# Optimization experiments

Measured on AMD Instinct MI355X. Metric: run time of the kernel, lower is better.

The kernel has to match this reference:

```python
import jax, jax.numpy as jnp
import numpy as np

N, E = 50000, 800000
IN, MAP, H, O = 256, 64, 4, 64
LEAKY_SLOPE = 0.2


def setup_inputs() -> dict:
    key = jax.random.key(0)
    ks = jax.random.split(key, 12)
    x = jax.random.normal(ks[0], (N, IN), dtype=jnp.float32)
    src = jax.random.randint(ks[1], (E,), 0, N, dtype=jnp.int32)
    dst = jax.random.randint(ks[2], (E,), 0, N, dtype=jnp.int32)
    s = 1.0 / np.sqrt(IN)
    W_gat = jax.random.normal(ks[3], (IN, H * O), dtype=jnp.float32) * s
    attn_l = jax.random.normal(ks[4], (H, O), dtype=jnp.float32) * 0.1
    attn_r = jax.random.normal(ks[5], (H, O), dtype=jnp.float32) * 0.1
    gate_m_W = jax.random.normal(ks[6], (IN, MAP), dtype=jnp.float32) * s
    gate_m_b = jnp.zeros((MAP,), dtype=jnp.float32)
    gate_fn_W = jax.random.normal(ks[7], (2 * IN + MAP, H), dtype=jnp.float32) * (1.0 / np.sqrt(2 * IN + MAP))
    gate_fn_b = jnp.zeros((H,), dtype=jnp.float32)
    merge_W = jax.random.normal(ks[8], (IN + O, O), dtype=jnp.float32) * (1.0 / np.sqrt(IN + O))
    merge_b = jnp.zeros((O,), dtype=jnp.float32)
    return {"x": x, "src": src, "dst": dst, "W_gat": W_gat, "attn_l": attn_l,
            "attn_r": attn_r, "gate_m_W": gate_m_W, "gate_m_b": gate_m_b,
            "gate_fn_W": gate_fn_W, "gate_fn_b": gate_fn_b,
            "merge_W": merge_W, "merge_b": merge_b}


def _forward(x, src, dst, W_gat, attn_l, attn_r, gate_m_W, gate_m_b,
             gate_fn_W, gate_fn_b, merge_W, merge_b):
    n = x.shape[0]
    # --- gate branch: gspmm mean of x, gspmm max of linear_z over in-neighbors ---
    deg = jax.ops.segment_sum(jnp.ones_like(dst, dtype=x.dtype), dst, num_segments=n)
    mean_z = jax.ops.segment_sum(x[src], dst, num_segments=n) / jnp.maximum(deg, 1.0)[:, None]
    z = x @ gate_m_W + gate_m_b  # [N, MAP]
    max_z = jax.ops.segment_max(z[src], dst, num_segments=n)
    max_z = jnp.where(deg[:, None] > 0, max_z, 0.0)  # empty neighborhoods -> 0
    nft = jnp.concatenate([x, max_z, mean_z], axis=1)  # [N, 2*IN+MAP]
    gate = jax.nn.sigmoid(nft @ gate_fn_W + gate_fn_b)  # [N, H]
    # --- GATConv ---
    feat = (x @ W_gat).reshape(n, H, O)  # [N, H, O]
    el = jnp.einsum('nho,ho->nh', feat, attn_l)
    er = jnp.einsum('nho,ho->nh', feat, attn_r)
    e = jax.nn.leaky_relu(el[src] + er[dst], negative_slope=LEAKY_SLOPE)  # [E, H]
    m = jax.ops.segment_max(e, dst, num_segments=n)  # [N, H]
    m = jnp.where(jnp.isfinite(m), m, 0.0)
    ex = jnp.exp(e - m[dst])  # [E, H]
    s = jax.ops.segment_sum(ex, dst, num_segments=n)  # [N, H]
    alpha = ex / jnp.maximum(s[dst], 1e-16)  # [E, H]
    attn_out = jax.ops.segment_sum(feat[src] * alpha[:, :, None], dst, num_segments=n)  # [N, H, O]
    # --- gated merge ---
    gated = (gate[:, :, None] * attn_out).mean(axis=1)  # [N, O]
    merge = jnp.concatenate([x, gated], axis=1) @ merge_W + merge_b  # [N, O]
    return merge


def reference(x, src, dst, W_gat, attn_l, attn_r, gate_m_W, gate_m_b,
              gate_fn_W, gate_fn_b, merge_W, merge_b):
    return _forward(x, src, dst, W_gat, attn_l, attn_r, gate_m_W, gate_m_b,
                    gate_fn_W, gate_fn_b, merge_W, merge_b)
```

## Files before the change

kernel.cpp:

```cpp
#include <hip/hip_runtime.h>
#include <math.h>

#define NN 50000
#define NE 800000
#define LEAKY 0.2f
#define NT 26
#define CAP 96
#define NBT (8 * NT * 64)

typedef short bf16x8 __attribute__((ext_vector_type(8)));
typedef float f32x4 __attribute__((ext_vector_type(4)));
typedef float f32x2 __attribute__((ext_vector_type(2)));

__device__ __forceinline__ unsigned short f2bf(float f) {
  unsigned u = __float_as_uint(f);
  u += 0x7fffu + ((u >> 16) & 1u);
  return (unsigned short)(u >> 16);
}
__device__ __forceinline__ float bf2f(unsigned short h) {
  return __uint_as_float((unsigned)h << 16);
}
__device__ __forceinline__ float leaky(float v) { return v > 0.0f ? v : LEAKY * v; }
__device__ __forceinline__ float rlf(float v, int l) {
  return __uint_as_float(__builtin_amdgcn_readlane(__float_as_uint(v), l));
}
__device__ __forceinline__ int rli(int v, int l) {
  return __builtin_amdgcn_readlane(v, l);
}

#if defined(__has_builtin)
#if __has_builtin(__builtin_amdgcn_cvt_pk_f32_fp8) && \
    __has_builtin(__builtin_amdgcn_cvt_pk_fp8_f32) && \
    __has_builtin(__builtin_amdgcn_cvt_f32_fp8)
#define FP8_HW 1
#endif
#endif

#ifdef FP8_HW
__device__ __forceinline__ unsigned char f2fp8(float v) {
  return (unsigned char)(__builtin_amdgcn_cvt_pk_fp8_f32(v, v, 0u, false) & 0xFF);
}
__device__ __forceinline__ f32x2 fp8x2_lo(unsigned int v) {
  return __builtin_amdgcn_cvt_pk_f32_fp8(v, false);
}
__device__ __forceinline__ f32x2 fp8x2_hi(unsigned int v) {
  return __builtin_amdgcn_cvt_pk_f32_fp8(v, true);
}
__device__ __forceinline__ float fp8one(unsigned int v) {
  return __builtin_amdgcn_cvt_f32_fp8(v, 0);
}
#else
__device__ __forceinline__ unsigned char f2fp8(float f) {
  unsigned u = __float_as_uint(f);
  unsigned s = (u >> 31) << 7;
  unsigned a = u & 0x7FFFFFFFu;
  if (a >= 0x43E00000u) return (unsigned char)(s | 0x7E);
  if (a < 0x3C800000u) {
    float m = __uint_as_float(a) * 512.0f;
    int q = (int)(m + 0.5f); if (q > 7) q = 7;
    return (unsigned char)(s | q);
  }
  a += 0x7FFFFu + ((a >> 20) & 1);
  unsigned e = ((a >> 23) & 0xFF) - 120;
  if (e > 15) return (unsigned char)(s | 0x7E);
  return (unsigned char)(s | (e << 3) | ((a >> 20) & 7));
}
__device__ __forceinline__ float fp8dec1(unsigned b) {
  unsigned s = (b & 0x80u) << 24;
  unsigned em = b & 0x7Fu;
  unsigned e4 = em >> 3, m3 = em & 7;
  float v = e4 ? __uint_as_float(((e4 + 120) << 23) | (m3 << 20))
               : (float)m3 * 0.001953125f;
  return __uint_as_float(__float_as_uint(v) ^ s);
}
__device__ __forceinline__ f32x2 fp8x2_lo(unsigned int v) {
  f32x2 r;
  r[0] = fp8dec1(v & 0xFF);
  r[1] = fp8dec1((v >> 8) & 0xFF);
  return r;
}
__device__ __forceinline__ f32x2 fp8x2_hi(unsigned int v) {
  f32x2 r;
  r[0] = fp8dec1((v >> 16) & 0xFF);
  r[1] = fp8dec1((v >> 24) & 0xFF);
  return r;
}
__device__ __forceinline__ float fp8one(unsigned int v) { return fp8dec1(v & 0xFF); }
#endif

__global__ void k_init(int* __restrict__ cursor, unsigned char* __restrict__ zq,
                       float* __restrict__ epay) {
  int i = blockIdx.x * 256 + threadIdx.x;
  if (i < NN) cursor[i] = 0;
  if (blockIdx.x == 0) {
    int t = threadIdx.x;
    if (t < 64) zq[(size_t)NN * 64 + t] = 0xFE;
    if (t < 8) epay[(size_t)NN * 8 + t] = 0.0f;
  }
}

__global__ void k_scatter(const int* __restrict__ src, const int* __restrict__ dst,
                          int* __restrict__ cursor, int* __restrict__ csr_src) {
  int e = blockIdx.x * 256 + threadIdx.x;
  if (e < NE) {
    int n = dst[e];
    int pos = atomicAdd(&cursor[n], 1);
    if (pos < CAP) csr_src[n * CAP + pos] = src[e];
  }
}

__device__ __forceinline__ float panel_w(int col, int k,
    const float* W_gat, const float* gate_m_W, const float* merge_W,
    const float* gate_fn_W) {
  if (col < 256)      return W_gat[k * 256 + (col & 3) * 64 + (col >> 2)];
  else if (col < 320) return gate_m_W[k * 64 + (col - 256)];
  else if (col < 384) return merge_W[k * 64 + (col - 320)];
  else if (col < 388) return gate_fn_W[k * 4 + (col - 384)];
  else if (col < 392) return gate_fn_W[(320 + k) * 4 + (col - 388)];
  return 0.0f;
}

__global__ void k_bt(const float* __restrict__ W_gat, const float* __restrict__ gate_m_W,
                     const float* __restrict__ merge_W, const float* __restrict__ gate_fn_W,
                     unsigned short* __restrict__ Btf, unsigned short* __restrict__ mWf) {
  int idx = blockIdx.x * 256 + threadIdx.x;
  if (idx < NBT) {
    int kq = idx / (NT * 64);
    int rem = idx - kq * (NT * 64);
    int t = rem >> 6, lane = rem & 63;
    int col = t * 16 + (lane & 15);
    int k = kq * 32 + (lane >> 4) * 8;
    unsigned short* o = Btf + (size_t)idx * 8;
#pragma unroll
    for (int i = 0; i < 8; ++i)
      o[i] = f2bf(panel_w(col, k + i, W_gat, gate_m_W, merge_W, gate_fn_W));
  } else if (idx < NBT + 512) {
    int idx2 = idx - NBT;
    int kq = idx2 >> 8;
    int rem = idx2 & 255;
    int t = rem >> 6, lane = rem & 63;
    int col = t * 16 + (lane & 15);
    int k = kq * 32 + ((lane >> 4) & 3) * 8;
    unsigned short* o = mWf + (size_t)idx2 * 8;
#pragma unroll
    for (int i = 0; i < 8; ++i)
      o[i] = f2bf(merge_W[(size_t)(256 + k + i) * 64 + col]);
  }
}

__global__ __launch_bounds__(256) void k_gemm_mfma(
    const float* __restrict__ x, const unsigned short* __restrict__ Btf,
    const float* __restrict__ gate_m_b,
    const float* __restrict__ attn_l, const float* __restrict__ attn_r,
    unsigned char* __restrict__ featq, unsigned char* __restrict__ zq,
    float* __restrict__ xm, float* __restrict__ gx, float* __restrict__ epay,
    float* __restrict__ erv) {
  __shared__ float els[32][4][2];
  __shared__ float ers[32][4][2];
  int lane = threadIdx.x & 63;
  int wave = threadIdx.x >> 6;
  int rowHalf = wave >> 1, colHalf = wave & 1;
  int rowB = blockIdx.x * 32;
  int row0 = rowB + rowHalf * 16;
  int t0 = colHalf * 13;
  int m = lane & 15;
  int kg = lane >> 4;
  f32x4 zero = {0.f, 0.f, 0.f, 0.f};
  f32x4 acc[13];
#pragma unroll
  for (int t = 0; t < 13; ++t) acc[t] = zero;
  int arow = row0 + m; if (arow >= NN) arow = NN - 1;
  const float* apf = x + (size_t)arow * 256 + kg * 8;
#pragma unroll 1
  for (int kq = 0; kq < 8; ++kq) {
    float4 fa = *(const float4*)(apf + kq * 32);
    float4 fb = *(const float4*)(apf + kq * 32 + 4);
    bf16x8 a;
    a[0] = (short)f2bf(fa.x); a[1] = (short)f2bf(fa.y);
    a[2] = (short)f2bf(fa.z); a[3] = (short)f2bf(fa.w);
    a[4] = (short)f2bf(fb.x); a[5] = (short)f2bf(fb.y);
    a[6] = (short)f2bf(fb.z); a[7] = (short)f2bf(fb.w);
    bf16x8 bfr[13];
#pragma unroll
    for (int t = 0; t < 13; ++t)
      bfr[t] = *(const bf16x8*)(Btf + (((size_t)kq * NT + t0 + t) * 64 + lane) * 8);
#pragma unroll
    for (int t = 0; t < 13; ++t)
      acc[t] = __builtin_amdgcn_mfma_f32_16x16x32_bf16(a, bfr[t], acc[t], 0, 0, 0);
  }

  int h = m & 3, od = m >> 2;
  float elp[4] = {0, 0, 0, 0}, erp[4] = {0, 0, 0, 0};
#pragma unroll
  for (int t = 0; t < 13; ++t) {
    if ((t0 + t) * 16 < 256) {
      int o = (t0 + t) * 4 + od;
      float al = attn_l[h * 64 + o];
      float ar = attn_r[h * 64 + o];
#pragma unroll
      for (int r = 0; r < 4; ++r) {
        elp[r] += acc[t][r] * al;
        erp[r] += acc[t][r] * ar;
      }
    }
  }
#pragma unroll
  for (int r = 0; r < 4; ++r) {
    elp[r] += __shfl_xor(elp[r], 4, 64); elp[r] += __shfl_xor(elp[r], 8, 64);
    erp[r] += __shfl_xor(erp[r], 4, 64); erp[r] += __shfl_xor(erp[r], 8, 64);
  }
  if (m < 4) {
#pragma unroll
    for (int r = 0; r < 4; ++r) {
      els[rowHalf * 16 + kg * 4 + r][m][colHalf] = elp[r];
      ers[rowHalf * 16 + kg * 4 + r][m][colHalf] = erp[r];
    }
  }

#pragma unroll
  for (int r = 0; r < 4; ++r) {
    int row = row0 + kg * 4 + r;
    if (row >= NN) continue;
#pragma unroll
    for (int t = 0; t < 13; ++t) {
      int c = (t0 + t) * 16 + m;
      float val = acc[t][r];
      if (c < 256) {
        featq[(size_t)row * 256 + c] = f2fp8(val);
      } else if (c < 320) {
        int cc = c - 256;
        zq[(size_t)row * 64 + cc] = f2fp8(val + gate_m_b[cc]);
      } else if (c < 384) {
        xm[(size_t)row * 64 + (c - 320)] = val;
      } else if (c < 388) {
        gx[(size_t)row * 4 + (c - 384)] = val;
      } else if (c < 392) {
        epay[(size_t)row * 8 + (c - 388) + 4] = val;
      }
    }
  }
  __syncthreads();
  int tid = threadIdx.x;
  if (tid < 128) {
    int rr = tid >> 2, h2 = tid & 3;
    int row = rowB + rr;
    if (row < NN) {
      epay[(size_t)row * 8 + h2] = els[rr][h2][0] + els[rr][h2][1];
      erv[(size_t)row * 4 + h2] = ers[rr][h2][0] + ers[rr][h2][1];
    }
  }
}

__global__ __launch_bounds__(256) void k_node(
    const unsigned char* __restrict__ zq, const unsigned char* __restrict__ featq,
    const float* __restrict__ epay, const float* __restrict__ er,
    const float* __restrict__ gx,
    const int* __restrict__ cursor, const int* __restrict__ csr_src,
    const float* __restrict__ gate_fn_W, const float* __restrict__ gate_fn_b,
    unsigned short* __restrict__ gatedb) {
  __shared__ float WzT[4][64];
  int tid = threadIdx.x;
  {
    int c = tid >> 2, h = tid & 3;
    WzT[h][c] = gate_fn_W[(256 + c) * 4 + h];
  }
  __syncthreads();

  int lane = tid & 63;
  int node = blockIdx.x * 4 + (tid >> 6);
  if (node >= NN) return;
  int deg = cursor[node]; if (deg > CAP) deg = CAP;
  if (deg == 0) {
    gatedb[(size_t)node * 64 + lane] = 0;
    return;
  }
  int rs = node * CAP, re = rs + deg;
  int hh = lane >> 4, le = lane & 15;
  float er_h = er[(size_t)node * 4 + hh];

  float a0 = 0, a1 = 0, a2 = 0, a3 = 0;
  float psum = 0, usum = 0;
  float mz = -INFINITY;
  for (int j0 = rs; j0 < re; j0 += 16) {
    int jj = j0 + le;
    bool valid = jj < re;
    int s_l = valid ? csr_src[jj] : NN;
    float el_v = epay[((size_t)(unsigned)s_l << 3) + hh];
    float u_v  = epay[((size_t)(unsigned)s_l << 3) + 4 + hh];
    float lg = leaky(el_v + er_h);
    float p = valid ? __expf(lg) : 0.0f;
    psum += p;
    usum += valid ? u_v : 0.0f;
#pragma unroll
    for (int e2 = 0; e2 < 16; ++e2) {
      int s = rli(s_l, e2);
      float p0 = rlf(p, e2);
      float p1 = rlf(p, e2 + 16);
      float p2 = rlf(p, e2 + 32);
      float p3 = rlf(p, e2 + 48);
      unsigned int fv = *(const unsigned int*)(featq + ((size_t)(unsigned)s << 8) + lane * 4);
      unsigned int zv = zq[((size_t)(unsigned)s << 6) + lane];
      f32x2 lo = fp8x2_lo(fv);
      f32x2 hi = fp8x2_hi(fv);
      a0 += p0 * lo[0];
      a1 += p1 * lo[1];
      a2 += p2 * hi[0];
      a3 += p3 * hi[1];
      mz = fmaxf(mz, fp8one(zv));
    }
  }
#pragma unroll
  for (int off = 1; off < 16; off <<= 1) {
    psum += __shfl_xor(psum, off, 64);
    usum += __shfl_xor(usum, off, 64);
  }
  float s0 = rlf(psum, 0),  s1 = rlf(psum, 16);
  float s2 = rlf(psum, 32), s3 = rlf(psum, 48);
  float su0 = rlf(usum, 0),  su1 = rlf(usum, 16);
  float su2 = rlf(usum, 32), su3 = rlf(usum, 48);

  float g[4];
#pragma unroll
  for (int h = 0; h < 4; ++h) {
    float t = mz * WzT[h][lane];
#pragma unroll
    for (int off = 32; off; off >>= 1) t += __shfl_xor(t, off, 64);
    g[h] = t;
  }
  float inv_deg = 1.0f / (float)deg;
  float4 gx4 = *(const float4*)(gx + (size_t)node * 4);
  float g0 = 1.0f / (1.0f + __expf(-(g[0] + gx4.x + su0 * inv_deg + gate_fn_b[0])));
  float g1 = 1.0f / (1.0f + __expf(-(g[1] + gx4.y + su1 * inv_deg + gate_fn_b[1])));
  float g2 = 1.0f / (1.0f + __expf(-(g[2] + gx4.z + su2 * inv_deg + gate_fn_b[2])));
  float g3 = 1.0f / (1.0f + __expf(-(g[3] + gx4.w + su3 * inv_deg + gate_fn_b[3])));

  float gated = 0.25f * (g0 * a0 / s0 + g1 * a1 / s1 + g2 * a2 / s2 + g3 * a3 / s3);
  gatedb[(size_t)node * 64 + lane] = f2bf(gated);
}

__global__ __launch_bounds__(256) void k_merge(
    const unsigned short* __restrict__ gatedb, const unsigned short* __restrict__ mWf,
    const float* __restrict__ xm, const float* __restrict__ merge_b,
    float* __restrict__ out) {
  int lane = threadIdx.x & 63;
  int wave = threadIdx.x >> 6;
  int row0 = blockIdx.x * 64 + wave * 16;
  int m = lane & 15;
  int kg = lane >> 4;
  f32x4 zero = {0.f, 0.f, 0.f, 0.f};
  f32x4 acc[4] = {zero, zero, zero, zero};
  int arow = row0 + m; if (arow >= NN) arow = NN - 1;
  const unsigned short* ap = gatedb + (size_t)arow * 64 + kg * 8;
#pragma unroll
  for (int kq = 0; kq < 2; ++kq) {
    bf16x8 a = *(const bf16x8*)(ap + kq * 32);
#pragma unroll
    for (int t = 0; t < 4; ++t) {
      bf16x8 b = *(const bf16x8*)(mWf + (((size_t)kq * 4 + t) * 64 + lane) * 8);
      acc[t] = __builtin_amdgcn_mfma_f32_16x16x32_bf16(a, b, acc[t], 0, 0, 0);
    }
  }
#pragma unroll
  for (int r = 0; r < 4; ++r) {
    int row = row0 + kg * 4 + r;
    if (row >= NN) continue;
#pragma unroll
    for (int t = 0; t < 4; ++t) {
      int c = t * 16 + m;
      out[(size_t)row * 64 + c] = acc[t][r] + xm[(size_t)row * 64 + c] + merge_b[c];
    }
  }
}

extern "C" void kernel_launch(void* const* d_in, const int* in_sizes, int n_in,
                              void* d_out, int out_size, void* d_ws, size_t ws_size,
                              hipStream_t stream) {
  const float* x         = (const float*)d_in[0];
  const int*   src       = (const int*)d_in[1];
  const int*   dst       = (const int*)d_in[2];
  const float* W_gat     = (const float*)d_in[3];
  const float* attn_l    = (const float*)d_in[4];
  const float* attn_r    = (const float*)d_in[5];
  const float* gate_m_W  = (const float*)d_in[6];
  const float* gate_m_b  = (const float*)d_in[7];
  const float* gate_fn_W = (const float*)d_in[8];
  const float* gate_fn_b = (const float*)d_in[9];
  const float* merge_W   = (const float*)d_in[10];
  const float* merge_b   = (const float*)d_in[11];
  float* out = (float*)d_out;

  char* ws = (char*)d_ws;
  size_t off = 0;
  auto alloc = [&](size_t bytes) -> void* {
    off = (off + 255) & ~(size_t)255;
    void* p = ws + off;
    off += bytes;
    return p;
  };
  int* cursor    = (int*)alloc((size_t)NN * 4);
  int* csr_src   = (int*)alloc((size_t)NN * CAP * 4);
  float* epay = (float*)alloc((size_t)(NN + 1) * 8 * 4);
  float* er   = (float*)alloc((size_t)NN * 4 * 4);
  float* gx   = (float*)alloc((size_t)NN * 4 * 4);
  float* xm   = (float*)alloc((size_t)NN * 64 * 4);
  unsigned char* zq    = (unsigned char*)alloc((size_t)(NN + 1) * 64);
  unsigned char* featq = (unsigned char*)alloc((size_t)(NN + 1) * 256);
  unsigned short* gatedb = (unsigned short*)alloc((size_t)NN * 64 * 2);
  unsigned short* Btf    = (unsigned short*)alloc((size_t)NBT * 8 * 2);
  unsigned short* mWf    = (unsigned short*)alloc((size_t)512 * 8 * 2);

  k_init<<<(NN + 255) / 256, 256, 0, stream>>>(cursor, zq, epay);
  k_scatter<<<(NE + 255) / 256, 256, 0, stream>>>(src, dst, cursor, csr_src);
  k_bt<<<(NBT + 512 + 255) / 256, 256, 0, stream>>>(W_gat, gate_m_W, merge_W, gate_fn_W,
                                                    Btf, mWf);
  k_gemm_mfma<<<(NN + 31) / 32, 256, 0, stream>>>(x, Btf, gate_m_b, attn_l, attn_r,
                                                  featq, zq, xm, gx, epay, er);
  k_node<<<(NN + 3) / 4, 256, 0, stream>>>(zq, featq, epay, er, gx, cursor, csr_src,
                                           gate_fn_W, gate_fn_b, gatedb);
  k_merge<<<(NN + 63) / 64, 256, 0, stream>>>(gatedb, mWf, xm, merge_b, out);
}
```

Measured before the change: 278.2 us.

## Pre-pack x into bf16 MFMA fragment layout and double-buffer GEMM operand loads

Adds a k_pack kernel that converts x to bf16 once, laid out in MFMA A-fragment order, so the GEMM loads ready 16-byte fragments instead of converting fp32 inline. The GEMM K-loop is unrolled by two with register double buffering of A and B fragments to overlap loads with MFMA. The epilogue is specialized per column half to remove per-element column branching. The cost is an extra kernel launch and an extra write and read of a 25MB bf16 copy of x. The last grid block reads an unwritten padding row block for out-of-range rows, but those results are not stored.

Result: faster. 268.4 us (-3.5%).

```diff
diff --git a/kernel.cpp b/kernel.cpp
--- a/kernel.cpp
+++ b/kernel.cpp
@@ -7,6 +7,7 @@
 #define NT 26
 #define CAP 96
 #define NBT (8 * NT * 64)
+#define NRB 3125
 
 typedef short bf16x8 __attribute__((ext_vector_type(8)));
 typedef float f32x4 __attribute__((ext_vector_type(4)));
@@ -107,6 +108,23 @@
     int pos = atomicAdd(&cursor[n], 1);
     if (pos < CAP) csr_src[n * CAP + pos] = src[e];
   }
+}
+
+__global__ __launch_bounds__(256) void k_pack(const float* __restrict__ x,
+                                              unsigned short* __restrict__ xf) {
+  int gid = blockIdx.x * 256 + threadIdx.x;
+  int rowblk = gid >> 9;
+  int rem = gid & 511;
+  int kq = rem >> 6, lane = rem & 63;
+  int m = lane & 15, kg = lane >> 4;
+  const float* p = x + (size_t)(rowblk * 16 + m) * 256 + kq * 32 + kg * 8;
+  float4 fa = *(const float4*)p;
+  float4 fb = *(const float4*)(p + 4);
+  ushort4 o0, o1;
+  o0.x = f2bf(fa.x); o0.y = f2bf(fa.y); o0.z = f2bf(fa.z); o0.w = f2bf(fa.w);
+  o1.x = f2bf(fb.x); o1.y = f2bf(fb.y); o1.z = f2bf(fb.z); o1.w = f2bf(fb.w);
+  ushort4* dst = (ushort4*)(xf + (size_t)gid * 8);
+  dst[0] = o0; dst[1] = o1;
 }
 
 __device__ __forceinline__ float panel_w(int col, int k,
@@ -149,7 +167,7 @@
 }
 
 __global__ __launch_bounds__(256) void k_gemm_mfma(
-    const float* __restrict__ x, const unsigned short* __restrict__ Btf,
+    const unsigned short* __restrict__ xf, const unsigned short* __restrict__ Btf,
     const float* __restrict__ gate_m_b,
     const float* __restrict__ attn_l, const float* __restrict__ attn_r,
     unsigned char* __restrict__ featq, unsigned char* __restrict__ zq,
@@ -169,24 +187,32 @@
   f32x4 acc[13];
 #pragma unroll
   for (int t = 0; t < 13; ++t) acc[t] = zero;
-  int arow = row0 + m; if (arow >= NN) arow = NN - 1;
-  const float* apf = x + (size_t)arow * 256 + kg * 8;
+
+  const unsigned short* aB = xf + ((size_t)(blockIdx.x * 2 + rowHalf) * 8 * 64 + lane) * 8;
+  const unsigned short* bB = Btf + (size_t)(t0 * 64 + lane) * 8;
+
+  bf16x8 a0, a1, b0[13], b1[13];
+  a0 = *(const bf16x8*)(aB);
+#pragma unroll
+  for (int t = 0; t < 13; ++t)
+    b0[t] = *(const bf16x8*)(bB + (size_t)t * 64 * 8);
 #pragma unroll 1
-  for (int kq = 0; kq < 8; ++kq) {
-    float4 fa = *(const float4*)(apf + kq * 32);
-    float4 fb = *(const float4*)(apf + kq * 32 + 4);
-    bf16x8 a;
-    a[0] = (short)f2bf(fa.x); a[1] = (short)f2bf(fa.y);
-    a[2] = (short)f2bf(fa.z); a[3] = (short)f2bf(fa.w);
-    a[4] = (short)f2bf(fb.x); a[5] = (short)f2bf(fb.y);
-    a[6] = (short)f2bf(fb.z); a[7] = (short)f2bf(fb.w);
-    bf16x8 bfr[13];
+  for (int kq = 0; kq < 8; kq += 2) {
+    a1 = *(const bf16x8*)(aB + (size_t)(kq + 1) * 64 * 8);
 #pragma unroll
     for (int t = 0; t < 13; ++t)
-      bfr[t] = *(const bf16x8*)(Btf + (((size_t)kq * NT + t0 + t) * 64 + lane) * 8);
+      b1[t] = *(const bf16x8*)(bB + ((size_t)(kq + 1) * NT + t) * 64 * 8);
 #pragma unroll
     for (int t = 0; t < 13; ++t)
-      acc[t] = __builtin_amdgcn_mfma_f32_16x16x32_bf16(a, bfr[t], acc[t], 0, 0, 0);
+      acc[t] = __builtin_amdgcn_mfma_f32_16x16x32_bf16(a0, b0[t], acc[t], 0, 0, 0);
+    int kq2 = kq + 2 < 8 ? kq + 2 : 7;
+    a0 = *(const bf16x8*)(aB + (size_t)kq2 * 64 * 8);
+#pragma unroll
+    for (int t = 0; t < 13; ++t)
+      b0[t] = *(const bf16x8*)(bB + ((size_t)kq2 * NT + t) * 64 * 8);
+#pragma unroll
+    for (int t = 0; t < 13; ++t)
+      acc[t] = __builtin_amdgcn_mfma_f32_16x16x32_bf16(a1, b1[t], acc[t], 0, 0, 0);
   }
 
   int h = m & 3, od = m >> 2;
@@ -217,26 +243,33 @@
     }
   }
 
-#pragma unroll
-  for (int r = 0; r < 4; ++r) {
-    int row = row0 + kg * 4 + r;
-    if (row >= NN) continue;
-#pragma unroll
-    for (int t = 0; t < 13; ++t) {
-      int c = (t0 + t) * 16 + m;
-      float val = acc[t][r];
-      if (c < 256) {
-        featq[(size_t)row * 256 + c] = f2fp8(val);
-      } else if (c < 320) {
-        int cc = c - 256;
-        zq[(size_t)row * 64 + cc] = f2fp8(val + gate_m_b[cc]);
-      } else if (c < 384) {
-        xm[(size_t)row * 64 + (c - 320)] = val;
-      } else if (c < 388) {
-        gx[(size_t)row * 4 + (c - 384)] = val;
-      } else if (c < 392) {
-        epay[(size_t)row * 8 + (c - 388) + 4] = val;
+  if (colHalf == 0) {
+#pragma unroll
+    for (int r = 0; r < 4; ++r) {
+      int row = row0 + kg * 4 + r;
+      if (row >= NN) continue;
+#pragma unroll
+      for (int t = 0; t < 13; ++t)
+        featq[(size_t)row * 256 + t * 16 + m] = f2fp8(acc[t][r]);
+    }
+  } else {
+#pragma unroll
+    for (int r = 0; r < 4; ++r) {
+      int row = row0 + kg * 4 + r;
+      if (row >= NN) continue;
+#pragma unroll
+      for (int t = 0; t < 3; ++t)
+        featq[(size_t)row * 256 + 208 + t * 16 + m] = f2fp8(acc[t][r]);
+#pragma unroll
+      for (int t = 3; t < 7; ++t) {
+        int cc = (t - 3) * 16 + m;
+        zq[(size_t)row * 64 + cc] = f2fp8(acc[t][r] + gate_m_b[cc]);
       }
+#pragma unroll
+      for (int t = 7; t < 11; ++t)
+        xm[(size_t)row * 64 + (t - 7) * 16 + m] = acc[t][r];
+      if (m < 4) gx[(size_t)row * 4 + m] = acc[11][r];
+      else if (m < 8) epay[(size_t)row * 8 + m] = acc[11][r];
     }
   }
   __syncthreads();
@@ -406,14 +439,16 @@
   unsigned char* zq    = (unsigned char*)alloc((size_t)(NN + 1) * 64);
   unsigned char* featq = (unsigned char*)alloc((size_t)(NN + 1) * 256);
   unsigned short* gatedb = (unsigned short*)alloc((size_t)NN * 64 * 2);
+  unsigned short* xf     = (unsigned short*)alloc((size_t)(NRB + 1) * 512 * 8 * 2);
   unsigned short* Btf    = (unsigned short*)alloc((size_t)NBT * 8 * 2);
   unsigned short* mWf    = (unsigned short*)alloc((size_t)512 * 8 * 2);
 
   k_init<<<(NN + 255) / 256, 256, 0, stream>>>(cursor, zq, epay);
   k_scatter<<<(NE + 255) / 256, 256, 0, stream>>>(src, dst, cursor, csr_src);
+  k_pack<<<(NRB * 512) / 256, 256, 0, stream>>>(x, xf);
   k_bt<<<(NBT + 512 + 255) / 256, 256, 0, stream>>>(W_gat, gate_m_W, merge_W, gate_fn_W,
                                                     Btf, mWf);
-  k_gemm_mfma<<<(NN + 31) / 32, 256, 0, stream>>>(x, Btf, gate_m_b, attn_l, attn_r,
+  k_gemm_mfma<<<(NN + 31) / 32, 256, 0, stream>>>(xf, Btf, gate_m_b, attn_l, attn_r,
                                                   featq, zq, xm, gx, epay, er);
   k_node<<<(NN + 3) / 4, 256, 0, stream>>>(zq, featq, epay, er, gx, cursor, csr_src,
                                            gate_fn_W, gate_fn_b, gatedb);
```
